# Kernel tuning notes

Measured on AMD Instinct MI355X. Metric: run time of the kernel, lower is better.

The kernel has to match this reference:

```python
import jax, jax.numpy as jnp
from jax import lax
import numpy as np

DIM = 64
HEADS = 4
R = 8  # reduction_ratio: kv conv kernel == stride == R


def setup_inputs() -> dict:
    key = jax.random.key(0)
    k_x, k_q, k_kv, k_o = jax.random.split(key, 4)
    x = jax.random.normal(k_x, (2, DIM, 32, 64, 64), dtype=jnp.float32)
    # 1x1x1 conv weights stored as [out_c, in_c]
    w_q = jax.random.normal(k_q, (DIM, DIM), dtype=jnp.float32) * (1.0 / np.sqrt(DIM))
    # strided kv conv weights: [out_c=2*dim, in_c=dim, R, R, R]
    fan_in = DIM * R * R * R
    w_kv = jax.random.normal(k_kv, (2 * DIM, DIM, R, R, R), dtype=jnp.float32) * (1.0 / np.sqrt(fan_in))
    w_out = jax.random.normal(k_o, (DIM, DIM), dtype=jnp.float32) * (1.0 / np.sqrt(DIM))
    return {"x": x, "w_q": w_q, "w_kv": w_kv, "w_out": w_out}


def _attn(x, w_q, w_kv, w_out):
    B, C, D, H, W = x.shape
    hd = C // HEADS  # per-head channel dim
    scale = hd ** (-0.5)

    # to_q: 1x1x1 conv == channel mixing
    q = jnp.einsum('oc,bcdhw->bodhw', w_q, x)
    # to_kv: conv3d kernel=stride=R, no padding
    kv = lax.conv_general_dilated(
        x, w_kv, window_strides=(R, R, R), padding='VALID',
        dimension_numbers=('NCDHW', 'OIDHW', 'NCDHW'))
    k, v = jnp.split(kv, 2, axis=1)  # each [B, C, D/R, H/R, W/R]

    def to_seq(t):
        # 'b (h c) d x y -> (b h) (d x y) c'
        b, c_all, d, h, w = t.shape
        t = t.reshape(b, HEADS, hd, d * h * w)
        return t.transpose(0, 1, 3, 2).reshape(b * HEADS, d * h * w, hd)

    qs, ks, vs = to_seq(q), to_seq(k), to_seq(v)  # [(B*H), N, c], [(B*H), Nr, c]

    sim = jnp.einsum('bic,bjc->bij', qs, ks) * scale  # [(B*H), N, Nr]
    attn = jax.nn.softmax(sim, axis=-1)
    out = jnp.einsum('bij,bjc->bic', attn, vs)  # [(B*H), N, c]

    # '(b h) (d x y) c -> b (h c) d x y'
    out = out.reshape(B, HEADS, D * H * W, hd).transpose(0, 1, 3, 2)
    out = out.reshape(B, C, D, H, W)
    return jnp.einsum('oc,bcdhw->bodhw', w_out, out)


def reference(x, w_q, w_kv, w_out):
    return _attn(x, w_q, w_kv, w_out)
```

## Files before the change

kernel.cpp:

```cpp
#include <hip/hip_runtime.h>
#include <hip/hip_bf16.h>

#define NPOS 131072

typedef __attribute__((ext_vector_type(8))) short short8;
typedef __attribute__((ext_vector_type(4))) float floatx4;
typedef unsigned int uint32;

__device__ __forceinline__ unsigned short bf16b(float v) {
    __hip_bfloat16 h = __float2bfloat16(v);
    return __builtin_bit_cast(unsigned short, h);
}
__device__ __forceinline__ uint32 cvtpk(float lo, float hi) {
    uint32 r;
    asm("v_cvt_pk_bf16_f32 %0, %1, %2" : "=v"(r) : "v"(lo), "v"(hi));
    return r;
}
__device__ __forceinline__ uint32 pkr(float lo, float hi) {
    uint32 ul = __builtin_bit_cast(uint32, lo) + 0x8000u;
    uint32 uh = __builtin_bit_cast(uint32, hi) + 0x8000u;
#if __has_builtin(__builtin_amdgcn_perm)
    return __builtin_amdgcn_perm(uh, ul, 0x07060302u);
#else
    return (uh & 0xFFFF0000u) | (ul >> 16);
#endif
}
__device__ __forceinline__ unsigned short bf16r(float v) {
    return (unsigned short)((__builtin_bit_cast(uint32, v) + 0x8000u) >> 16);
}
#if __has_builtin(__builtin_amdgcn_exp2f)
#define EXP2(x) __builtin_amdgcn_exp2f(x)
#else
#define EXP2(x) exp2f(x)
#endif
#if __has_builtin(__builtin_amdgcn_rcpf)
#define RCPF(x) __builtin_amdgcn_rcpf(x)
#else
#define RCPF(x) (1.0f / (x))
#endif

__device__ __forceinline__ short8 emb4(uint32 w0, uint32 w1) {
    union { uint32 u[4]; short8 s; } z;
    z.u[0] = w0; z.u[1] = w1; z.u[2] = 0; z.u[3] = 0;
    return z.s;
}
__device__ __forceinline__ short8 emb4m(const unsigned short* p) {
    uint32 w[2];
    __builtin_memcpy(w, p, 8);
    return emb4(w[0], w[1]);
}
__device__ __forceinline__ short8 mk8(uint32 a, uint32 b, uint32 c, uint32 d) {
    union { uint32 u[4]; short8 s; } z;
    z.u[0] = a; z.u[1] = b; z.u[2] = c; z.u[3] = d;
    return z.s;
}

__global__ void k_prep_w(const float* __restrict__ wq, const float* __restrict__ wout,
                         unsigned short* __restrict__ wqb, unsigned short* __restrict__ woutb) {
    const float QS = 0.36067376022224085f;
    int gid = blockIdx.x * 256 + threadIdx.x;
    wqb[gid]   = bf16b(wq[gid] * QS);
    woutb[gid] = bf16b(wout[gid]);
}

__global__ void k_prep_wkvb(const float* __restrict__ wkv, unsigned short* __restrict__ wtb) {
    int gid = blockIdx.x * 256 + threadIdx.x;
    int ic = gid >> 14;
    int oc = (gid >> 7) & 127;
    float4 v = *(const float4*)(wkv + ((size_t)(oc * 64 + ic)) * 512 + (size_t)(gid & 127) * 4);
    uint32* dst = (uint32*)(wtb + (size_t)gid * 4);
    dst[0] = cvtpk(v.x, v.y);
    dst[1] = cvtpk(v.z, v.w);
}

__global__ __launch_bounds__(256) void k_conv_mfma(const float* __restrict__ x,
                                                   const unsigned short* __restrict__ wtb,
                                                   float* __restrict__ partial) {
    __shared__ __align__(16) unsigned short As[64 * 72];
    __shared__ __align__(16) unsigned short Bs[128 * 72];
    const int bid = blockIdx.x;
    const int ic = bid & 63;
    const int b  = (bid >> 6) & 1;
    const int pz = bid >> 7;
    const int tid = threadIdx.x;
    const int lane = tid & 63, wv = tid >> 6;
    const int lc = lane & 15, lg = lane >> 4;

    floatx4 acc[4][2];
#pragma unroll
    for (int mt = 0; mt < 4; ++mt)
#pragma unroll
        for (int n = 0; n < 2; ++n) acc[mt][n] = {0.f, 0.f, 0.f, 0.f};

    const float* xp = x + ((size_t)b * 64 + ic) * NPOS + (size_t)pz * 8 * 4096;
    const unsigned short* wp = wtb + (size_t)ic * 128 * 512;

    for (int rz = 0; rz < 8; ++rz) {
        __syncthreads();
        const float* plane = xp + (size_t)rz * 4096;
#pragma unroll
        for (int t2 = 0; t2 < 4; ++t2) {
            int e = (t2 * 256 + tid) * 4;
            int y = e >> 6, x0 = e & 63;
            int p = ((y >> 3) << 3) + (x0 >> 3);
            int k = ((y & 7) << 3) + (x0 & 7);
            float4 v = *(const float4*)(plane + e);
            uint32* dst = (uint32*)&As[p * 72 + k];
            dst[0] = cvtpk(v.x, v.y);
            dst[1] = cvtpk(v.z, v.w);
        }
        {
            int oc = tid >> 1, hf = tid & 1;
            const uint4* src = (const uint4*)(wp + (size_t)oc * 512 + rz * 64 + hf * 32);
            uint4* dst = (uint4*)&Bs[oc * 72 + hf * 32];
#pragma unroll
            for (int r = 0; r < 4; ++r) dst[r] = src[r];
        }
        __syncthreads();
#pragma unroll
        for (int ks = 0; ks < 2; ++ks) {
            short8 bb0 = *(const short8*)&Bs[((wv * 2 + 0) * 16 + lc) * 72 + ks * 32 + lg * 8];
            short8 bb1 = *(const short8*)&Bs[((wv * 2 + 1) * 16 + lc) * 72 + ks * 32 + lg * 8];
#pragma unroll
            for (int mt = 0; mt < 4; ++mt) {
                short8 a = *(const short8*)&As[(mt * 16 + lc) * 72 + ks * 32 + lg * 8];
                acc[mt][0] = __builtin_amdgcn_mfma_f32_16x16x32_bf16(a, bb0, acc[mt][0], 0, 0, 0);
                acc[mt][1] = __builtin_amdgcn_mfma_f32_16x16x32_bf16(a, bb1, acc[mt][1], 0, 0, 0);
            }
        }
    }
    float* pb = partial + (((size_t)ic * 2 + b) * 256 + pz * 64) * 128;
#pragma unroll
    for (int mt = 0; mt < 4; ++mt)
#pragma unroll
        for (int ntl = 0; ntl < 2; ++ntl) {
            int oc = (wv * 2 + ntl) * 16 + lc;
#pragma unroll
            for (int r = 0; r < 4; ++r) {
                int m = mt * 16 + lg * 4 + r;
                pb[(size_t)m * 128 + oc] = acc[mt][ntl][r];
            }
        }
}

__global__ void k_reduce(const float* __restrict__ partial,
                         unsigned short* __restrict__ kt, unsigned short* __restrict__ vt) {
    int gid = blockIdx.x * 256 + threadIdx.x;
    int oc = gid & 127;
    int bp = gid >> 7;
    int b = bp >> 8;
    int j = bp & 255;
    const float* p = partial + (size_t)bp * 128 + oc;
    float s = 0.f;
#pragma unroll 8
    for (int ic = 0; ic < 64; ++ic) s += p[(size_t)ic * 65536];
    int h = (oc & 63) >> 4, i = oc & 15;
    if (oc < 64) {
        kt[(((size_t)b * 4 + h) * 256 + j) * 16 + i] = bf16b(s);
    } else {
        int q = j & 31;
        int jp = (j & ~31) | (((q & 15) >> 2) * 8 + (q & 3) + ((q >> 4) << 2));
        vt[(((size_t)b * 4 + h) * 16 + i) * 256 + jp] = bf16b(s);
    }
}

__global__ __launch_bounds__(256, 5) void k_attn16(
    const float* __restrict__ x, const unsigned short* __restrict__ wqb,
    const unsigned short* __restrict__ woutb, const unsigned short* __restrict__ kt,
    const unsigned short* __restrict__ vt, float* __restrict__ out)
{
    __shared__ __align__(16) unsigned short s_at[64 * 72];
    __shared__ __align__(16) unsigned short s_q[4][64 * 20];

    const int tid = threadIdx.x;
    const int b = blockIdx.x >> 11;
    const int n_base = (blockIdx.x & 2047) << 6;
    const int lane = tid & 63;
    const int wv = tid >> 6;
    const int lc = lane & 15;
    const int lg = lane >> 4;

    unsigned short* qs = s_q[wv];

    {
        int n_l = tid & 63;
        int c0  = (tid >> 6) * 16;
        const float* xb = x + ((size_t)b << 23) + n_base + n_l;
        uint32* xrow = (uint32*)&s_at[n_l * 72 + c0];
#pragma unroll
        for (int r = 0; r < 8; ++r) {
            float v0 = xb[(size_t)(c0 + 2 * r) << 17];
            float v1 = xb[(size_t)(c0 + 2 * r + 1) << 17];
            xrow[r] = cvtpk(v0, v1);
        }
    }
    __syncthreads();

#pragma unroll
    for (int t = 0; t < 4; ++t) {
        floatx4 c = {0.f, 0.f, 0.f, 0.f};
#pragma unroll
        for (int ks = 0; ks < 2; ++ks) {
            short8 a = *(const short8*)&s_at[(t * 16 + lc) * 72 + ks * 32 + lg * 8];
            short8 bfull;
            __builtin_memcpy(&bfull, wqb + (wv * 16 + lc) * 64 + ks * 32 + lg * 8, 16);
            c = __builtin_amdgcn_mfma_f32_16x16x32_bf16(a, bfull, c, 0, 0, 0);
        }
#pragma unroll
        for (int r = 0; r < 4; ++r)
            qs[(t * 16 + lg * 4 + r) * 20 + lc] = bf16b(c[r]);
    }

    __syncthreads();

    short8 qf[4];
#pragma unroll
    for (int t = 0; t < 4; ++t)
        qf[t] = emb4m(&qs[(t * 16 + lc) * 20 + lg * 4]);

    const unsigned short* kbase = kt + (((size_t)b * 4 + wv) << 12) + lc * 16 + lg * 4;
    const unsigned short* vbase = vt + (((size_t)b * 4 + wv) << 12) + lc * 256 + lg * 8;
    const short8 ONES = {(short)0x3F80, (short)0x3F80, (short)0x3F80, (short)0x3F80,
                         (short)0x3F80, (short)0x3F80, (short)0x3F80, (short)0x3F80};
    const floatx4 Z = {0.f, 0.f, 0.f, 0.f};
    floatx4 pv[4], pvl[4];
#pragma unroll
    for (int t = 0; t < 4; ++t) { pv[t] = Z; pvl[t] = Z; }

#pragma unroll
    for (int m = 0; m < 8; ++m) {
        short8 kf0 = emb4m(kbase + m * 512);
        short8 kf1 = emb4m(kbase + m * 512 + 256);
        short8 vf;
        __builtin_memcpy(&vf, vbase + m * 32, 16);
#pragma unroll
        for (int t = 0; t < 4; ++t) {
            floatx4 c0 = __builtin_amdgcn_mfma_f32_16x16x32_bf16(kf0, qf[t], Z, 0, 0, 0);
            floatx4 c1 = __builtin_amdgcn_mfma_f32_16x16x32_bf16(kf1, qf[t], Z, 0, 0, 0);
            float p0 = EXP2(c0[0]), p1 = EXP2(c0[1]), p2 = EXP2(c0[2]), p3 = EXP2(c0[3]);
            float p4 = EXP2(c1[0]), p5 = EXP2(c1[1]), p6 = EXP2(c1[2]), p7 = EXP2(c1[3]);
            short8 pa = mk8(pkr(p0, p1), pkr(p2, p3), pkr(p4, p5), pkr(p6, p7));
            pv[t]  = __builtin_amdgcn_mfma_f32_16x16x32_bf16(pa, vf,   pv[t],  0, 0, 0);
            pvl[t] = __builtin_amdgcn_mfma_f32_16x16x32_bf16(pa, ONES, pvl[t], 0, 0, 0);
        }
    }

#pragma unroll
    for (int t = 0; t < 4; ++t) {
#pragma unroll
        for (int r = 0; r < 4; ++r) {
            float rl = RCPF(pvl[t][r]);
            s_at[(t * 16 + lg * 4 + r) * 72 + wv * 16 + lc] = bf16r(pv[t][r] * rl);
        }
    }

    __syncthreads();

#pragma unroll
    for (int t = 0; t < 4; ++t) {
        floatx4 c = {0.f, 0.f, 0.f, 0.f};
#pragma unroll
        for (int ks = 0; ks < 2; ++ks) {
            short8 a = *(const short8*)&s_at[(t * 16 + lc) * 72 + ks * 32 + lg * 8];
            short8 bfull;
            __builtin_memcpy(&bfull, woutb + (wv * 16 + lc) * 64 + ks * 32 + lg * 8, 16);
            c = __builtin_amdgcn_mfma_f32_16x16x32_bf16(a, bfull, c, 0, 0, 0);
        }
        float* dst = out + ((size_t)b << 23) + (size_t)(wv * 16 + lc) * NPOS
                   + n_base + t * 16 + lg * 4;
        *(floatx4*)dst = c;
    }
}

extern "C" void kernel_launch(void* const* d_in, const int* in_sizes, int n_in,
                              void* d_out, int out_size, void* d_ws, size_t ws_size,
                              hipStream_t stream) {
    const float* x    = (const float*)d_in[0];
    const float* wq   = (const float*)d_in[1];
    const float* wkv  = (const float*)d_in[2];
    const float* wout = (const float*)d_in[3];
    float* out = (float*)d_out;
    float* ws = (float*)d_ws;

    unsigned short* wtb = (unsigned short*)ws;
    float* partial = ws + 2097152;
    unsigned short* ktu = (unsigned short*)(ws + 6291456);
    unsigned short* vtu   = ktu + 32768;
    unsigned short* wqb   = vtu + 32768;
    unsigned short* woutb = wqb + 4096;

    k_prep_w   <<<16,   256, 0, stream>>>(wq, wout, wqb, woutb);
    k_prep_wkvb<<<4096, 256, 0, stream>>>(wkv, wtb);
    k_conv_mfma<<<512,  256, 0, stream>>>(x, wtb, partial);
    k_reduce   <<<256,  256, 0, stream>>>(partial, ktu, vtu);
    k_attn16   <<<4096, 256, 0, stream>>>(x, wqb, woutb, ktu, vtu, out);
}
```

Before: 87.67 us.

## Fuse weight bf16 conversion into conv and reduce kernels, drop prep launches

Removes the two separate weight-preparation kernels. The conv kernel now reads fp32 kv weights directly and converts them to bf16 while filling shared memory, and the q/out weight conversion moves into the reduce kernel. This saves two launches plus the write and re-read of a bf16 weight buffer of about 8 MB. In exchange, each conv block reads fp32 weights, twice the bytes of bf16, and repeats the conversion. That cost is multiplied across the 8 pz blocks that share each weight slice.

```diff
diff --git a/kernel.cpp b/kernel.cpp
--- a/kernel.cpp
+++ b/kernel.cpp
@@ -55,26 +55,8 @@
     return z.s;
 }
 
-__global__ void k_prep_w(const float* __restrict__ wq, const float* __restrict__ wout,
-                         unsigned short* __restrict__ wqb, unsigned short* __restrict__ woutb) {
-    const float QS = 0.36067376022224085f;
-    int gid = blockIdx.x * 256 + threadIdx.x;
-    wqb[gid]   = bf16b(wq[gid] * QS);
-    woutb[gid] = bf16b(wout[gid]);
-}
-
-__global__ void k_prep_wkvb(const float* __restrict__ wkv, unsigned short* __restrict__ wtb) {
-    int gid = blockIdx.x * 256 + threadIdx.x;
-    int ic = gid >> 14;
-    int oc = (gid >> 7) & 127;
-    float4 v = *(const float4*)(wkv + ((size_t)(oc * 64 + ic)) * 512 + (size_t)(gid & 127) * 4);
-    uint32* dst = (uint32*)(wtb + (size_t)gid * 4);
-    dst[0] = cvtpk(v.x, v.y);
-    dst[1] = cvtpk(v.z, v.w);
-}
-
 __global__ __launch_bounds__(256) void k_conv_mfma(const float* __restrict__ x,
-                                                   const unsigned short* __restrict__ wtb,
+                                                   const float* __restrict__ wkv,
                                                    float* __restrict__ partial) {
     __shared__ __align__(16) unsigned short As[64 * 72];
     __shared__ __align__(16) unsigned short Bs[128 * 72];
@@ -93,7 +75,8 @@
         for (int n = 0; n < 2; ++n) acc[mt][n] = {0.f, 0.f, 0.f, 0.f};
 
     const float* xp = x + ((size_t)b * 64 + ic) * NPOS + (size_t)pz * 8 * 4096;
-    const unsigned short* wp = wtb + (size_t)ic * 128 * 512;
+    const int oc = tid >> 1, hf = tid & 1;
+    const float* wsrc = wkv + ((size_t)(oc * 64 + ic)) * 512 + hf * 32;
 
     for (int rz = 0; rz < 8; ++rz) {
         __syncthreads();
@@ -110,11 +93,14 @@
             dst[1] = cvtpk(v.z, v.w);
         }
         {
-            int oc = tid >> 1, hf = tid & 1;
-            const uint4* src = (const uint4*)(wp + (size_t)oc * 512 + rz * 64 + hf * 32);
-            uint4* dst = (uint4*)&Bs[oc * 72 + hf * 32];
-#pragma unroll
-            for (int r = 0; r < 4; ++r) dst[r] = src[r];
+            const float4* s4 = (const float4*)(wsrc + rz * 64);
+            uint32* d = (uint32*)&Bs[oc * 72 + hf * 32];
+#pragma unroll
+            for (int r = 0; r < 8; ++r) {
+                float4 v = s4[r];
+                d[2 * r]     = cvtpk(v.x, v.y);
+                d[2 * r + 1] = cvtpk(v.z, v.w);
+            }
         }
         __syncthreads();
 #pragma unroll
@@ -134,18 +120,25 @@
     for (int mt = 0; mt < 4; ++mt)
 #pragma unroll
         for (int ntl = 0; ntl < 2; ++ntl) {
-            int oc = (wv * 2 + ntl) * 16 + lc;
+            int oco = (wv * 2 + ntl) * 16 + lc;
 #pragma unroll
             for (int r = 0; r < 4; ++r) {
                 int m = mt * 16 + lg * 4 + r;
-                pb[(size_t)m * 128 + oc] = acc[mt][ntl][r];
+                pb[(size_t)m * 128 + oco] = acc[mt][ntl][r];
             }
         }
 }
 
 __global__ void k_reduce(const float* __restrict__ partial,
-                         unsigned short* __restrict__ kt, unsigned short* __restrict__ vt) {
+                         const float* __restrict__ wq, const float* __restrict__ wout,
+                         unsigned short* __restrict__ kt, unsigned short* __restrict__ vt,
+                         unsigned short* __restrict__ wqb, unsigned short* __restrict__ woutb) {
     int gid = blockIdx.x * 256 + threadIdx.x;
+    if (gid < 4096) {
+        const float QS = 0.36067376022224085f;
+        wqb[gid]   = bf16b(wq[gid] * QS);
+        woutb[gid] = bf16b(wout[gid]);
+    }
     int oc = gid & 127;
     int bp = gid >> 7;
     int b = bp >> 8;
@@ -282,16 +275,13 @@
     float* out = (float*)d_out;
     float* ws = (float*)d_ws;
 
-    unsigned short* wtb = (unsigned short*)ws;
-    float* partial = ws + 2097152;
-    unsigned short* ktu = (unsigned short*)(ws + 6291456);
+    float* partial = ws;
+    unsigned short* ktu   = (unsigned short*)(ws + 4194304);
     unsigned short* vtu   = ktu + 32768;
     unsigned short* wqb   = vtu + 32768;
     unsigned short* woutb = wqb + 4096;
 
-    k_prep_w   <<<16,   256, 0, stream>>>(wq, wout, wqb, woutb);
-    k_prep_wkvb<<<4096, 256, 0, stream>>>(wkv, wtb);
-    k_conv_mfma<<<512,  256, 0, stream>>>(x, wtb, partial);
-    k_reduce   <<<256,  256, 0, stream>>>(partial, ktu, vtu);
+    k_conv_mfma<<<512,  256, 0, stream>>>(x, wkv, partial);
+    k_reduce   <<<256,  256, 0, stream>>>(partial, wq, wout, ktu, vtu, wqb, woutb);
     k_attn16   <<<4096, 256, 0, stream>>>(x, wqb, woutb, ktu, vtu, out);
 }
```

Result: no change. 87.47 us (-0.2%).
